# Kernel tuning notes

Measured on AMD Instinct MI355X. Metric: run time of the kernel, lower is better.

## Reference

```python
import jax, jax.numpy as jnp
import numpy as np

N_NODES = 8192
N_EDGES = 49152
IN_F, HID, H1, H2, OUT_F = 128, 64, 64, 5, 32
N_BONDS = 64


def setup_inputs() -> dict:
    key = jax.random.key(0)
    ks = jax.random.split(key, 12)
    s = 0.05
    return {
        "x": jax.random.normal(ks[0], (N_NODES, IN_F), jnp.float32),
        "edge_index": jax.random.randint(ks[1], (2, N_EDGES), 0, N_NODES, jnp.int32),
        "lefts": jax.random.randint(ks[2], (N_BONDS,), 0, N_NODES, jnp.int32),
        "rights": jax.random.randint(ks[3], (N_BONDS,), 0, N_NODES, jnp.int32),
        "W1": jax.random.normal(ks[4], (H1 * HID, IN_F), jnp.float32) * s,
        "att_src1": jax.random.normal(ks[5], (H1, HID), jnp.float32) * s,
        "att_dst1": jax.random.normal(ks[6], (H1, HID), jnp.float32) * s,
        "b1": jnp.zeros((H1 * HID,), jnp.float32),
        "W2": jax.random.normal(ks[7], (H2 * OUT_F, H1 * HID), jnp.float32) * s,
        "att_src2": jax.random.normal(ks[8], (H2, OUT_F), jnp.float32) * s,
        "att_dst2": jax.random.normal(ks[9], (H2, OUT_F), jnp.float32) * s,
        "b2": jnp.zeros((OUT_F,), jnp.float32),
    }


def _gat_conv(x, src, dst, W, a_src, a_dst, b, concat):
    # x: [N, F_in]; W: [H*C, F_in]; a_src/a_dst: [H, C]
    N = x.shape[0]
    H, C = a_src.shape
    h = (x @ W.T).reshape(N, H, C)                    # [N, H, C]
    alpha_s = jnp.einsum("nhc,hc->nh", h, a_src)      # [N, H]
    alpha_d = jnp.einsum("nhc,hc->nh", h, a_dst)
    logits = jax.nn.leaky_relu(alpha_s[src] + alpha_d[dst], negative_slope=0.2)  # [E, H]
    # scatter-softmax over incoming edges of each destination node
    m = jax.ops.segment_max(logits, dst, num_segments=N)
    e = jnp.exp(logits - m[dst])
    denom = jax.ops.segment_sum(e, dst, num_segments=N)
    alpha = e / denom[dst]                            # [E, H]
    msg = h[src] * alpha[:, :, None]                  # [E, H, C]
    out = jax.ops.segment_sum(msg, dst, num_segments=N)  # [N, H, C]
    out = out.reshape(N, H * C) if concat else out.mean(axis=1)
    return out + b


def reference(x, edge_index, lefts, rights, W1, att_src1, att_dst1, b1,
              W2, att_src2, att_dst2, b2):
    N = x.shape[0]
    loops = jnp.arange(N, dtype=edge_index.dtype)
    src = jnp.concatenate([edge_index[0], loops])
    dst = jnp.concatenate([edge_index[1], loops])
    x1 = jax.nn.elu(_gat_conv(x, src, dst, W1, att_src1, att_dst1, b1, concat=True))
    x2 = _gat_conv(x1, src, dst, W2, att_src2, att_dst2, b2, concat=False)  # [N, OUT_F]
    score = (x2[lefts] + x2[rights]).sum(axis=-1)     # [N_BONDS]
    return jax.nn.softmax(score, axis=0)
```

## Files before the change

### kernel.cpp

```cpp
#include <hip/hip_runtime.h>
#include <hip/hip_bf16.h>
#include <math.h>

#define N_NODES  8192
#define N_EDGES  49152
#define E_TOT    57344
#define IN_F     128
#define HID      64
#define NH1      64
#define NH2      5
#define OUT_F    32
#define F1       4096
#define F2       160
#define N_BONDS  64
#define ET       16
#define NP       4
#define HG       16

typedef short bf16x8 __attribute__((ext_vector_type(8)));
typedef float f32x4  __attribute__((ext_vector_type(4)));

__device__ __forceinline__ float lrelu(float x){ return x > 0.f ? x : 0.2f*x; }

__device__ __forceinline__ unsigned short bf16_rne(float f){
    unsigned u = __float_as_uint(f);
    unsigned r = u + 0x7FFF + ((u >> 16) & 1);
    return (unsigned short)(r >> 16);
}
__device__ __forceinline__ float bf16f(unsigned short h){
    return __uint_as_float((unsigned)h << 16);
}

__device__ __forceinline__ void block_sync_lds(){
    asm volatile("s_waitcnt lgkmcnt(0)" ::: "memory");
    __builtin_amdgcn_s_barrier();
    asm volatile("" ::: "memory");
}

__device__ __forceinline__ void gload_lds16(const unsigned short* gp, unsigned short* lp_base){
    __builtin_amdgcn_global_load_lds(
        (const __attribute__((address_space(1))) unsigned int*)(const void*)gp,
        (__attribute__((address_space(3))) unsigned int*)(void*)lp_base,
        16, 0, 0);
}

__global__ void k_init_counts(int* counts){
    int i = blockIdx.x*256 + threadIdx.x;
    if (i < N_NODES) counts[i] = 1;
}
__global__ void k_count(const int* __restrict__ ei, int* counts){
    int i = blockIdx.x*256 + threadIdx.x;
    if (i < N_EDGES) atomicAdd(&counts[ei[N_EDGES + i]], 1);
}
__global__ __launch_bounds__(1024) void k_scan(const int* __restrict__ counts,
                                               int* __restrict__ row_start,
                                               int* __restrict__ cursor){
    __shared__ int sd[1024];
    int t = threadIdx.x;
    int v[8]; int sum = 0;
    #pragma unroll
    for (int i=0;i<8;i++){ v[i] = counts[t*8+i]; sum += v[i]; }
    sd[t] = sum; __syncthreads();
    for (int off=1; off<1024; off<<=1){
        int vv = (t >= off) ? sd[t-off] : 0;
        __syncthreads();
        sd[t] += vv;
        __syncthreads();
    }
    int run = sd[t] - sum;
    #pragma unroll
    for (int i=0;i<8;i++){ row_start[t*8+i] = run; cursor[t*8+i] = run; run += v[i]; }
    if (t == 1023) row_start[N_NODES] = run;
}
__global__ void k_fill(const int* __restrict__ ei, int* cursor, int* __restrict__ csr_src){
    int i = blockIdx.x*256 + threadIdx.x;
    if (i >= E_TOT) return;
    int s, d;
    if (i < N_EDGES){ s = ei[i]; d = ei[N_EDGES + i]; }
    else { s = i - N_EDGES; d = s; }
    int pos = atomicAdd(&cursor[d], 1);
    csr_src[pos] = s;
}

__global__ void k_packw1d(const float* __restrict__ W1,
                          unsigned short* __restrict__ fh, unsigned short* __restrict__ fl){
    int g = blockIdx.x*256 + threadIdx.x;
    int lane = g & 63, ct = (g >> 6) & 3, ks = (g >> 8) & 3, hg = g >> 10;
    int col = hg*64 + ct*16 + (lane & 15);
    int k = ks*32 + (lane >> 4)*8;
    const float* src = W1 + (size_t)col*IN_F + k;
    bf16x8 hv, lv;
    #pragma unroll
    for (int j=0;j<8;j++){
        float f = src[j];
        unsigned short hb = bf16_rne(f);
        hv[j] = (short)hb;
        lv[j] = (short)bf16_rne(f - bf16f(hb));
    }
    *(bf16x8*)(fh + (size_t)g*8) = hv;
    *(bf16x8*)(fl + (size_t)g*8) = lv;
}

__global__ void k_packw2d(const float* __restrict__ W2,
                          unsigned short* __restrict__ fh, unsigned short* __restrict__ fl){
    int g = blockIdx.x*256 + threadIdx.x;
    int lane = g & 63, ni = (g >> 6) % 10, kc = g / 640;
    int n = ni*16 + (lane & 15);
    int k = kc*32 + (lane >> 4)*8;
    const float* src = W2 + (size_t)n*F1 + k;
    bf16x8 hv, lv;
    #pragma unroll
    for (int j=0;j<8;j++){
        float f = src[j];
        unsigned short hb = bf16_rne(f);
        hv[j] = (short)hb;
        lv[j] = (short)bf16_rne(f - bf16f(hb));
    }
    *(bf16x8*)(fh + (size_t)g*8) = hv;
    *(bf16x8*)(fl + (size_t)g*8) = lv;
}

__global__ __launch_bounds__(128) void k_attvec(const float* __restrict__ W1,
        const float* __restrict__ a_s, const float* __restrict__ a_d,
        float* __restrict__ vsT, float* __restrict__ vdT){
    int h = blockIdx.x, k = threadIdx.x;
    float s = 0.f, d = 0.f;
    for (int c = 0; c < HID; c++){
        float w = W1[(size_t)(h*HID + c)*IN_F + k];
        s += a_s[h*HID + c] * w;
        d += a_d[h*HID + c] * w;
    }
    vsT[k*NH1 + h] = s;
    vdT[k*NH1 + h] = d;
}

__global__ __launch_bounds__(128) void k_alpha1x(const float* __restrict__ x,
        const float* __restrict__ vsT, const float* __restrict__ vdT,
        float* __restrict__ as1, float* __restrict__ ad1){
    int n = blockIdx.x, t = threadIdx.x;
    __shared__ float xs[IN_F];
    xs[t] = x[(size_t)n*IN_F + t];
    __syncthreads();
    if (t < NH1){
        float s = 0.f, d = 0.f;
        for (int k = 0; k < IN_F; k++){
            float xv = xs[k];
            s += xv * vsT[k*NH1 + t];
            d += xv * vdT[k*NH1 + t];
        }
        as1[n*NH1 + t] = s;
        ad1[n*NH1 + t] = d;
    }
}

__global__ __launch_bounds__(256) void k_aggx64(const float* __restrict__ x,
        const float* __restrict__ as1, const float* __restrict__ ad1,
        const int* __restrict__ row_start, const int* __restrict__ csr_src,
        unsigned short* __restrict__ txhi){
    int n = blockIdx.x, t = threadIdx.x;
    __shared__ float ad_s[NH1];
    __shared__ float wt[ET][NH1];
    __shared__ int   st[ET];
    __shared__ float xs[ET][IN_F];
    int e0 = row_start[n], e1 = row_start[n+1];
    if (t < NH1) ad_s[t] = ad1[n*NH1 + t];
    int hq = t >> 4, f0 = (t & 15)*8;
    float acc[4][8] = {};
    float D[4] = {0.f, 0.f, 0.f, 0.f};
    for (int eb = e0; eb < e1; eb += ET){
        int ne = min(ET, e1 - eb);
        if (t < ne) st[t] = csr_src[eb + t];
        __syncthreads();
        for (int idx = t; idx < ne*32; idx += 256){
            int e = idx >> 5, f4 = idx & 31;
            *(float4*)&xs[e][f4*4] = *(const float4*)(x + (size_t)st[e]*IN_F + f4*4);
        }
        for (int idx = t; idx < ne*NH1; idx += 256){
            int e = idx >> 6, hh = idx & 63;
            wt[e][hh] = expf(lrelu(as1[st[e]*NH1 + hh] + ad_s[hh]));
        }
        __syncthreads();
        for (int e = 0; e < ne; e++){
            float4 v0 = *(const float4*)&xs[e][f0];
            float4 v1 = *(const float4*)&xs[e][f0+4];
            float xv[8] = {v0.x,v0.y,v0.z,v0.w,v1.x,v1.y,v1.z,v1.w};
            #pragma unroll
            for (int c=0;c<4;c++){
                float w = wt[e][hq*4 + c];
                D[c] += w;
                #pragma unroll
                for (int j=0;j<8;j++) acc[c][j] += w*xv[j];
            }
        }
        __syncthreads();
    }
    #pragma unroll
    for (int c=0;c<4;c++){
        float dinv = 1.f / D[c];
        bf16x8 hv;
        #pragma unroll
        for (int j=0;j<8;j++) hv[j] = (short)bf16_rne(acc[c][j] * dinv);
        size_t o = ((size_t)(hq*4 + c)*N_NODES + n)*IN_F + f0;
        *(bf16x8*)(txhi + o) = hv;
    }
}

__global__ __launch_bounds__(512, 4) void k_gemm12(
        const unsigned short* __restrict__ txhi,
        const unsigned short* __restrict__ w1fh, const unsigned short* __restrict__ w1fl,
        const unsigned short* __restrict__ w2fh, const unsigned short* __restrict__ w2fl,
        const float* __restrict__ b1,
        float* __restrict__ P){
    __shared__ __attribute__((aligned(16))) unsigned short Als[8192];
    __shared__ __attribute__((aligned(16))) unsigned short W1sh[8192];
    __shared__ __attribute__((aligned(16))) unsigned short W2s[20480];
    __shared__ __attribute__((aligned(16))) unsigned short X1s[4096];

    const int tid  = threadIdx.x;
    const int wave = tid >> 6, lane = tid & 63;
    const int wr = wave >> 1, wc = wave & 1;
    const int q = lane >> 4, l16 = lane & 15;
    const int row0 = blockIdx.x * 64;
    const int g = blockIdx.y;
    const int h0 = g * HG;

    {
        const unsigned short* Ab = txhi + ((size_t)h0*N_NODES + row0)*IN_F;
        const unsigned short* W1b = w1fh + (size_t)h0*8192;
        #pragma unroll
        for (int j=0;j<2;j++){
            int idx = j*8 + wave;
            int eo = idx*512 + lane*8;
            int row = eo >> 7;
            int se = (eo & ~127) | ((eo & 127) ^ ((row & 7) << 3));
            gload_lds16(Ab + se, &Als[idx*512]);
        }
        #pragma unroll
        for (int j=0;j<2;j++){
            int idx = j*8 + wave;
            gload_lds16(W1b + idx*512 + lane*8, &W1sh[idx*512]);
        }
    }

    f32x4 acc2[5] = {};
    bf16x8 wlo[8];

    #pragma unroll 1
    for (int hh = 0; hh < HG; hh++){
        const int h = h0 + hh;
        block_sync_lds();
        {
            const unsigned short* W2bh = w2fh + (size_t)h*10240;
            const unsigned short* W2bl = w2fl + (size_t)h*10240;
            #pragma unroll
            for (int j=0;j<5;j++){
                int idx = j*8 + wave;
                const unsigned short* src = (idx < 20) ? (W2bh + idx*512 + lane*8)
                                                       : (W2bl + (idx-20)*512 + lane*8);
                gload_lds16(src, &W2s[idx*512]);
            }
        }
        asm volatile("" ::: "memory");
        {
            const unsigned short* W1lb = w1fl + (size_t)h*8192;
            #pragma unroll
            for (int ks=0;ks<4;ks++)
                #pragma unroll
                for (int ni=0;ni<2;ni++)
                    wlo[ks*2+ni] = *(const bf16x8*)(W1lb + (size_t)(ks*4 + 2*wc + ni)*512 + lane*8);
        }
        asm volatile("s_waitcnt vmcnt(8)" ::: "memory");
        __builtin_amdgcn_s_barrier();
        const int arow = wr*16 + l16;
        f32x4 c1[2] = {};
        #pragma unroll
        for (int ks=0;ks<4;ks++){
            int sidx = (arow*128 + ks*32 + q*8) ^ ((arow & 7) << 3);
            bf16x8 af = *(const bf16x8*)&Als[sidx];
            #pragma unroll
            for (int ni=0;ni<2;ni++){
                bf16x8 bh = *(const bf16x8*)&W1sh[(ks*4 + 2*wc + ni)*512 + lane*8];
                c1[ni] = __builtin_amdgcn_mfma_f32_16x16x32_bf16(af, bh, c1[ni], 0,0,0);
                c1[ni] = __builtin_amdgcn_mfma_f32_16x16x32_bf16(af, wlo[ks*2+ni], c1[ni], 0,0,0);
            }
        }
        #pragma unroll
        for (int ni=0;ni<2;ni++){
            int col = (2*wc+ni)*16 + l16;
            float b = b1[h*64 + col];
            #pragma unroll
            for (int i=0;i<4;i++){
                float v = c1[ni][i] + b;
                float o = v > 0.f ? v : expm1f(v);
                int row = wr*16 + q*4 + i;
                int sidx = (row*64 + col) ^ ((row & 7) << 3);
                X1s[sidx] = bf16_rne(o);
            }
        }
        block_sync_lds();
        if (hh + 1 < HG){
            const unsigned short* Ab = txhi + ((size_t)(h+1)*N_NODES + row0)*IN_F;
            const unsigned short* W1b = w1fh + (size_t)(h+1)*8192;
            #pragma unroll
            for (int j=0;j<2;j++){
                int idx = j*8 + wave;
                int eo = idx*512 + lane*8;
                int row = eo >> 7;
                int se = (eo & ~127) | ((eo & 127) ^ ((row & 7) << 3));
                gload_lds16(Ab + se, &Als[idx*512]);
            }
            #pragma unroll
            for (int j=0;j<2;j++){
                int idx = j*8 + wave;
                gload_lds16(W1b + idx*512 + lane*8, &W1sh[idx*512]);
            }
        }
        const int xrow = wr*16 + l16;
        #pragma unroll
        for (int ks=0;ks<2;ks++){
            int sidx = (xrow*64 + ks*32 + q*8) ^ ((xrow & 7) << 3);
            bf16x8 a2 = *(const bf16x8*)&X1s[sidx];
            #pragma unroll
            for (int ni=0;ni<5;ni++){
                int f = (ks*10 + wc*5 + ni)*512 + lane*8;
                bf16x8 bh = *(const bf16x8*)&W2s[f];
                bf16x8 bl = *(const bf16x8*)&W2s[10240 + f];
                acc2[ni] = __builtin_amdgcn_mfma_f32_16x16x32_bf16(a2, bh, acc2[ni], 0,0,0);
                acc2[ni] = __builtin_amdgcn_mfma_f32_16x16x32_bf16(a2, bl, acc2[ni], 0,0,0);
            }
        }
    }

    float* outp = P + ((size_t)g*N_NODES + row0)*F2;
    #pragma unroll
    for (int ni=0;ni<5;ni++)
        #pragma unroll
        for (int i=0;i<4;i++){
            int rr = wr*16 + q*4 + i;
            int cc = wc*80 + ni*16 + l16;
            outp[(size_t)rr*F2 + cc] = acc2[ni][i];
        }
}

__global__ __launch_bounds__(256) void k_reduce(const float* __restrict__ P,
                                                float* __restrict__ h2){
    const int NV = N_NODES*F2/4;
    int i = blockIdx.x*256 + threadIdx.x;
    float4 a = ((const float4*)P)[i];
    #pragma unroll
    for (int kb = 1; kb < NP; kb++){
        float4 b = ((const float4*)P)[(size_t)kb*NV + i];
        a.x += b.x; a.y += b.y; a.z += b.z; a.w += b.w;
    }
    ((float4*)h2)[i] = a;
}

__global__ __launch_bounds__(64) void k_alpha2(const float* __restrict__ h2,
        const float* __restrict__ att_s, const float* __restrict__ att_d,
        float* __restrict__ as2, float* __restrict__ ad2){
    int n = blockIdx.x, t = threadIdx.x;
    float ps = 0.f, pd = 0.f;
    if (t < 40){
        float4 h = *(const float4*)(h2 + (size_t)n*F2 + t*4);
        float4 a = ((const float4*)att_s)[t];
        float4 d = ((const float4*)att_d)[t];
        ps = h.x*a.x + h.y*a.y + h.z*a.z + h.w*a.w;
        pd = h.x*d.x + h.y*d.y + h.z*d.z + h.w*d.w;
    }
    ps += __shfl_xor(ps,1); ps += __shfl_xor(ps,2); ps += __shfl_xor(ps,4);
    pd += __shfl_xor(pd,1); pd += __shfl_xor(pd,2); pd += __shfl_xor(pd,4);
    if (t < 40 && (t & 7) == 0){
        as2[n*NH2 + (t>>3)] = ps;
        ad2[n*NH2 + (t>>3)] = pd;
    }
}

__global__ __launch_bounds__(256) void k_agg2(const float* __restrict__ h2,
        const float* __restrict__ as2, const float* __restrict__ ad2,
        const int* __restrict__ row_start, const int* __restrict__ csr_src,
        const float* __restrict__ b2, float* __restrict__ x2){
    int n = blockIdx.x, t = threadIdx.x;
    __shared__ float ad_s[NH2], den_s[NH2], sacc[F2];
    int e0 = row_start[n], e1 = row_start[n+1];
    if (t < NH2) ad_s[t] = ad2[n*NH2 + t];
    __syncthreads();
    if (t < NH2){
        float d = 0.f;
        for (int e=e0;e<e1;e++){
            int s = csr_src[e];
            d += expf(lrelu(as2[s*NH2 + t] + ad_s[t]));
        }
        den_s[t] = d;
    }
    __syncthreads();
    if (t < F2){
        int h = t >> 5;
        float adh  = ad_s[h];
        float dinv = 1.f/den_s[h];
        float acc = 0.f;
        for (int e=e0;e<e1;e++){
            int s = csr_src[e];
            float w = expf(lrelu(as2[s*NH2 + h] + adh)) * dinv;
            acc += w * h2[(size_t)s*F2 + t];
        }
        sacc[t] = acc;
    }
    __syncthreads();
    if (t < OUT_F){
        float v = (sacc[t] + sacc[t+32] + sacc[t+64] + sacc[t+96] + sacc[t+128]) * 0.2f + b2[t];
        x2[n*OUT_F + t] = v;
    }
}

__global__ __launch_bounds__(64) void k_bond(const float* __restrict__ x2,
        const int* __restrict__ lefts, const int* __restrict__ rights,
        float* __restrict__ out){
    int b = threadIdx.x;
    int L = lefts[b], R = rights[b];
    float s = 0.f;
    #pragma unroll
    for (int c=0;c<OUT_F;c+=4){
        float4 l4 = *(const float4*)(x2 + (size_t)L*OUT_F + c);
        float4 r4 = *(const float4*)(x2 + (size_t)R*OUT_F + c);
        s += l4.x+l4.y+l4.z+l4.w + r4.x+r4.y+r4.z+r4.w;
    }
    float m = s;
    #pragma unroll
    for (int off=1; off<64; off<<=1) m = fmaxf(m, __shfl_xor(m, off));
    float e = expf(s - m);
    float sum = e;
    #pragma unroll
    for (int off=1; off<64; off<<=1) sum += __shfl_xor(sum, off);
    out[b] = e / sum;
}

extern "C" void kernel_launch(void* const* d_in, const int* in_sizes, int n_in,
                              void* d_out, int out_size, void* d_ws, size_t ws_size,
                              hipStream_t stream){
    const float* x      = (const float*)d_in[0];
    const int*   ei     = (const int*)  d_in[1];
    const int*   lefts  = (const int*)  d_in[2];
    const int*   rights = (const int*)  d_in[3];
    const float* W1     = (const float*)d_in[4];
    const float* att_s1 = (const float*)d_in[5];
    const float* att_d1 = (const float*)d_in[6];
    const float* b1     = (const float*)d_in[7];
    const float* W2     = (const float*)d_in[8];
    const float* att_s2 = (const float*)d_in[9];
    const float* att_d2 = (const float*)d_in[10];
    const float* b2     = (const float*)d_in[11];
    float* out = (float*)d_out;

    char* ws = (char*)d_ws;
    size_t off = 0;
    auto alloc = [&](size_t bytes) -> void* {
        void* p = ws + off;
        off += (bytes + 255) & ~(size_t)255;
        return p;
    };
    unsigned short* txhi = (unsigned short*)alloc((size_t)NH1*N_NODES*IN_F*2);
    float* part   = (float*)alloc((size_t)NP*N_NODES*F2*4);
    float* h2     = (float*)alloc((size_t)N_NODES*F2*4);
    float* as1    = (float*)alloc((size_t)N_NODES*NH1*4);
    float* ad1    = (float*)alloc((size_t)N_NODES*NH1*4);
    float* as2    = (float*)alloc((size_t)N_NODES*NH2*4);
    float* ad2    = (float*)alloc((size_t)N_NODES*NH2*4);
    float* x2     = (float*)alloc((size_t)N_NODES*OUT_F*4);
    float* vsT    = (float*)alloc((size_t)IN_F*NH1*4);
    float* vdT    = (float*)alloc((size_t)IN_F*NH1*4);
    unsigned short* w1fh = (unsigned short*)alloc((size_t)F1*IN_F*2);
    unsigned short* w1fl = (unsigned short*)alloc((size_t)F1*IN_F*2);
    unsigned short* w2fh = (unsigned short*)alloc((size_t)128*10*512*2);
    unsigned short* w2fl = (unsigned short*)alloc((size_t)128*10*512*2);
    int* counts    = (int*)alloc((size_t)N_NODES*4);
    int* row_start = (int*)alloc((size_t)(N_NODES+1)*4);
    int* cursor    = (int*)alloc((size_t)N_NODES*4);
    int* csr_src   = (int*)alloc((size_t)E_TOT*4);

    k_init_counts<<<32, 256, 0, stream>>>(counts);
    k_count<<<192, 256, 0, stream>>>(ei, counts);
    k_scan<<<1, 1024, 0, stream>>>(counts, row_start, cursor);
    k_fill<<<224, 256, 0, stream>>>(ei, cursor, csr_src);

    k_packw1d<<<65536/256, 256, 0, stream>>>(W1, w1fh, w1fl);
    k_packw2d<<<81920/256, 256, 0, stream>>>(W2, w2fh, w2fl);

    k_attvec<<<NH1, 128, 0, stream>>>(W1, att_s1, att_d1, vsT, vdT);
    k_alpha1x<<<N_NODES, 128, 0, stream>>>(x, vsT, vdT, as1, ad1);

    k_aggx64<<<N_NODES, 256, 0, stream>>>(x, as1, ad1, row_start, csr_src, txhi);

    k_gemm12<<<dim3(128, NP), 512, 0, stream>>>(txhi, w1fh, w1fl, w2fh, w2fl, b1, part);
    k_reduce<<<N_NODES*F2/4/256, 256, 0, stream>>>(part, h2);

    k_alpha2<<<N_NODES, 64, 0, stream>>>(h2, att_s2, att_d2, as2, ad2);
    k_agg2<<<N_NODES, 256, 0, stream>>>(h2, as2, ad2, row_start, csr_src, b2, x2);

    k_bond<<<1, 64, 0, stream>>>(x2, lefts, rights, out);
}
```

Baseline: 258.3 us.

## Fuse partial reduction with layer-2 attention scores, use fast exp, tune gemm scheduling

Merges the split-K partial-sum reduction and the alpha2 computation into a single kernel that stages 64 nodes' h2 rows in LDS, removing one launch and a reread of h2. Replaces expf/expm1f with __expf in the aggregation and ELU paths. In the fused GEMM kernel it issues the W1-low register loads before the W2 LDS copies, adjusts the vmcnt wait, replaces one LDS sync with an explicit wait and barrier, and raises wave priority around the MFMA loops. Fast exp lowers accuracy slightly, and the fused reduce kernel runs only 128 blocks, so it has less parallelism.

Result: faster. 241.7 us (-6.4%).

```diff
diff --git a/kernel.cpp b/kernel.cpp
--- a/kernel.cpp
+++ b/kernel.cpp
@@ -177,7 +177,7 @@
         }
         for (int idx = t; idx < ne*NH1; idx += 256){
             int e = idx >> 6, hh = idx & 63;
-            wt[e][hh] = expf(lrelu(as1[st[e]*NH1 + hh] + ad_s[hh]));
+            wt[e][hh] = __expf(lrelu(as1[st[e]*NH1 + hh] + ad_s[hh]));
         }
         __syncthreads();
         for (int e = 0; e < ne; e++){
@@ -250,6 +250,15 @@
         const int h = h0 + hh;
         block_sync_lds();
         {
+            const unsigned short* W1lb = w1fl + (size_t)h*8192;
+            #pragma unroll
+            for (int ks=0;ks<4;ks++)
+                #pragma unroll
+                for (int ni=0;ni<2;ni++)
+                    wlo[ks*2+ni] = *(const bf16x8*)(W1lb + (size_t)(ks*4 + 2*wc + ni)*512 + lane*8);
+        }
+        asm volatile("" ::: "memory");
+        {
             const unsigned short* W2bh = w2fh + (size_t)h*10240;
             const unsigned short* W2bl = w2fl + (size_t)h*10240;
             #pragma unroll
@@ -260,19 +269,11 @@
                 gload_lds16(src, &W2s[idx*512]);
             }
         }
-        asm volatile("" ::: "memory");
-        {
-            const unsigned short* W1lb = w1fl + (size_t)h*8192;
-            #pragma unroll
-            for (int ks=0;ks<4;ks++)
-                #pragma unroll
-                for (int ni=0;ni<2;ni++)
-                    wlo[ks*2+ni] = *(const bf16x8*)(W1lb + (size_t)(ks*4 + 2*wc + ni)*512 + lane*8);
-        }
-        asm volatile("s_waitcnt vmcnt(8)" ::: "memory");
+        asm volatile("s_waitcnt vmcnt(13)" ::: "memory");
         __builtin_amdgcn_s_barrier();
         const int arow = wr*16 + l16;
         f32x4 c1[2] = {};
+        __builtin_amdgcn_s_setprio(1);
         #pragma unroll
         for (int ks=0;ks<4;ks++){
             int sidx = (arow*128 + ks*32 + q*8) ^ ((arow & 7) << 3);
@@ -284,6 +285,7 @@
                 c1[ni] = __builtin_amdgcn_mfma_f32_16x16x32_bf16(af, wlo[ks*2+ni], c1[ni], 0,0,0);
             }
         }
+        __builtin_amdgcn_s_setprio(0);
         #pragma unroll
         for (int ni=0;ni<2;ni++){
             int col = (2*wc+ni)*16 + l16;
@@ -291,13 +293,14 @@
             #pragma unroll
             for (int i=0;i<4;i++){
                 float v = c1[ni][i] + b;
-                float o = v > 0.f ? v : expm1f(v);
+                float o = v > 0.f ? v : (__expf(v) - 1.f);
                 int row = wr*16 + q*4 + i;
                 int sidx = (row*64 + col) ^ ((row & 7) << 3);
                 X1s[sidx] = bf16_rne(o);
             }
         }
-        block_sync_lds();
+        asm volatile("s_waitcnt vmcnt(0) lgkmcnt(0)" ::: "memory");
+        __builtin_amdgcn_s_barrier();
         if (hh + 1 < HG){
             const unsigned short* Ab = txhi + ((size_t)(h+1)*N_NODES + row0)*IN_F;
             const unsigned short* W1b = w1fh + (size_t)(h+1)*8192;
@@ -316,6 +319,7 @@
             }
         }
         const int xrow = wr*16 + l16;
+        __builtin_amdgcn_s_setprio(1);
         #pragma unroll
         for (int ks=0;ks<2;ks++){
             int sidx = (xrow*64 + ks*32 + q*8) ^ ((xrow & 7) << 3);
@@ -329,6 +333,7 @@
                 acc2[ni] = __builtin_amdgcn_mfma_f32_16x16x32_bf16(a2, bl, acc2[ni], 0,0,0);
             }
         }
+        __builtin_amdgcn_s_setprio(0);
     }
 
     float* outp = P + ((size_t)g*N_NODES + row0)*F2;
@@ -342,36 +347,41 @@
         }
 }
 
-__global__ __launch_bounds__(256) void k_reduce(const float* __restrict__ P,
-                                                float* __restrict__ h2){
+__global__ __launch_bounds__(256) void k_redalpha(const float* __restrict__ P,
+        const float* __restrict__ att_s, const float* __restrict__ att_d,
+        float* __restrict__ h2, float* __restrict__ as2, float* __restrict__ ad2){
+    __shared__ float hs[64][164];
+    __shared__ float avs[160], avd[160];
+    int b = blockIdx.x, t = threadIdx.x;
+    int n0 = b*64;
+    if (t < 160){ avs[t] = att_s[t]; avd[t] = att_d[t]; }
     const int NV = N_NODES*F2/4;
-    int i = blockIdx.x*256 + threadIdx.x;
-    float4 a = ((const float4*)P)[i];
-    #pragma unroll
-    for (int kb = 1; kb < NP; kb++){
-        float4 b = ((const float4*)P)[(size_t)kb*NV + i];
-        a.x += b.x; a.y += b.y; a.z += b.z; a.w += b.w;
-    }
-    ((float4*)h2)[i] = a;
-}
-
-__global__ __launch_bounds__(64) void k_alpha2(const float* __restrict__ h2,
-        const float* __restrict__ att_s, const float* __restrict__ att_d,
-        float* __restrict__ as2, float* __restrict__ ad2){
-    int n = blockIdx.x, t = threadIdx.x;
-    float ps = 0.f, pd = 0.f;
-    if (t < 40){
-        float4 h = *(const float4*)(h2 + (size_t)n*F2 + t*4);
-        float4 a = ((const float4*)att_s)[t];
-        float4 d = ((const float4*)att_d)[t];
-        ps = h.x*a.x + h.y*a.y + h.z*a.z + h.w*a.w;
-        pd = h.x*d.x + h.y*d.y + h.z*d.z + h.w*d.w;
-    }
-    ps += __shfl_xor(ps,1); ps += __shfl_xor(ps,2); ps += __shfl_xor(ps,4);
-    pd += __shfl_xor(pd,1); pd += __shfl_xor(pd,2); pd += __shfl_xor(pd,4);
-    if (t < 40 && (t & 7) == 0){
-        as2[n*NH2 + (t>>3)] = ps;
-        ad2[n*NH2 + (t>>3)] = pd;
+    int base = b * (64*F2/4);
+    #pragma unroll
+    for (int v=0; v<10; v++){
+        int i = base + v*256 + t;
+        float4 a = ((const float4*)P)[i];
+        #pragma unroll
+        for (int kb=1; kb<NP; kb++){
+            float4 bb = ((const float4*)P)[(size_t)kb*NV + i];
+            a.x+=bb.x; a.y+=bb.y; a.z+=bb.z; a.w+=bb.w;
+        }
+        ((float4*)h2)[i] = a;
+        int flat = (v*256 + t)*4;
+        int n = flat / F2, c = flat % F2;
+        *(float4*)&hs[n][c] = a;
+    }
+    __syncthreads();
+    for (int idx = t; idx < 320; idx += 256){
+        int n = idx/5, hh = idx%5;
+        const float* hp = &hs[n][hh*32];
+        const float* ap = &avs[hh*32];
+        const float* dp = &avd[hh*32];
+        float s=0.f, d=0.f;
+        #pragma unroll
+        for (int c=0;c<32;c++){ float hv=hp[c]; s += hv*ap[c]; d += hv*dp[c]; }
+        as2[(n0+n)*NH2 + hh] = s;
+        ad2[(n0+n)*NH2 + hh] = d;
     }
 }
 
@@ -388,7 +398,7 @@
         float d = 0.f;
         for (int e=e0;e<e1;e++){
             int s = csr_src[e];
-            d += expf(lrelu(as2[s*NH2 + t] + ad_s[t]));
+            d += __expf(lrelu(as2[s*NH2 + t] + ad_s[t]));
         }
         den_s[t] = d;
     }
@@ -400,7 +410,7 @@
         float acc = 0.f;
         for (int e=e0;e<e1;e++){
             int s = csr_src[e];
-            float w = expf(lrelu(as2[s*NH2 + h] + adh)) * dinv;
+            float w = __expf(lrelu(as2[s*NH2 + h] + adh)) * dinv;
             acc += w * h2[(size_t)s*F2 + t];
         }
         sacc[t] = acc;
@@ -491,9 +501,8 @@
     k_aggx64<<<N_NODES, 256, 0, stream>>>(x, as1, ad1, row_start, csr_src, txhi);
 
     k_gemm12<<<dim3(128, NP), 512, 0, stream>>>(txhi, w1fh, w1fl, w2fh, w2fl, b1, part);
-    k_reduce<<<N_NODES*F2/4/256, 256, 0, stream>>>(part, h2);
-
-    k_alpha2<<<N_NODES, 64, 0, stream>>>(h2, att_s2, att_d2, as2, ad2);
+    k_redalpha<<<128, 256, 0, stream>>>(part, att_s2, att_d2, h2, as2, ad2);
+
     k_agg2<<<N_NODES, 256, 0, stream>>>(h2, as2, ad2, row_start, csr_src, b2, x2);
 
     k_bond<<<1, 64, 0, stream>>>(x2, lefts, rights, out);
```
